# Optimization experiments

Measured on AMD Instinct MI355X. Metric: run time of the kernel, lower is better.

The kernel has to match this reference:

```python
import jax, jax.numpy as jnp
import numpy as np

H = 224          # image height (self.shape[0])
W_IMG = 224      # image width (self.shape[1])
CELLS = 7        # mask_generator num_cells
PAD = CELLS // 2 # reflect pad size
D = 512          # encoder feature dim
NUM_BATCHES = 30
BATCH = 100
EPS = 1e-8       # torch CosineSimilarity eps


def _encode(xb, Wenc):
    # stand-in encoder: 32x32 block average pool -> [B,3,7,7] -> linear to D
    B = xb.shape[0]
    feats = xb.reshape(B, 3, CELLS, H // CELLS, CELLS, W_IMG // CELLS).mean(axis=(3, 5))
    return feats.reshape(B, -1) @ Wenc  # [B, D]


def _cosine(a, b):
    # a: [1,D] (h_star), b: [B,D]; matches nn.CosineSimilarity(dim=1)
    num = jnp.sum(a * b, axis=1)
    den = jnp.maximum(jnp.linalg.norm(a, axis=1) * jnp.linalg.norm(b, axis=1), EPS)
    return num / den  # [B]


def _make_masks(grid, sx, sy):
    # grid: [B,1,7,7] binary floats; bilinear upsample, reflect pad, shifted crop
    B = grid.shape[0]
    up = jax.image.resize(grid, (B, 1, H, W_IMG), method='linear')
    padded = jnp.pad(up, ((0, 0), (0, 0), (PAD, PAD), (PAD, PAD)), mode='reflect')
    crop = jax.vmap(
        lambda g, i, j: jax.lax.dynamic_slice(g, (0, i, j), (1, H, W_IMG))
    )(padded, sx, sy)
    return crop  # [B,1,H,W]


def _relax(x, Wenc, grids, shifts_x, shifts_y):
    h_star = _encode(x, Wenc)  # [1, D]
    R0 = jnp.zeros((H, W_IMG), jnp.float32)
    U0 = jnp.zeros_like(R0)
    sow0 = jnp.full((H, W_IMG), 1e-10, jnp.float32)

    def sample_step(carry, inp):
        # sequential weighted running-mean / Welford variance update
        R, U, sow = carry
        s, m = inp  # s: scalar sim, m: [H,W] mask
        sow = sow + m
        R_new = R + m * (s - R) / sow
        U = U + (s - R_new) * (s - R) * m
        return (R_new, U, sow), None

    def batch_step(carry, binp):
        grid, sx, sy = binp
        masks = _make_masks(grid, sx, sy)        # [B,1,H,W]
        x_mask = x * masks                       # fill_vals_zeros=True path
        h = _encode(x_mask, Wenc)                # [B,D]
        sims = _cosine(h_star, h)                # [B]
        carry, _ = jax.lax.scan(sample_step, carry, (sims, masks[:, 0]))
        return carry, None

    (R, U, sow), _ = jax.lax.scan(batch_step, (R0, U0, sow0),
                                  (grids, shifts_x, shifts_y))
    uncertainty = U / (sow - 1.0)
    return jnp.stack([R, uncertainty])  # [2,H,W]: importance, uncertainty


def setup_inputs() -> dict:
    key = jax.random.key(0)
    k1, k2, k3, k4, k5 = jax.random.split(key, 5)
    x = jax.random.normal(k1, (1, 3, H, W_IMG), jnp.float32)
    Wenc = jax.random.normal(k2, (3 * CELLS * CELLS, D), jnp.float32) * 0.05
    grids = (jax.random.uniform(k3, (NUM_BATCHES, BATCH, 1, CELLS, CELLS)) < 0.5).astype(jnp.float32)
    shifts_x = jax.random.randint(k4, (NUM_BATCHES, BATCH), 0, CELLS)
    shifts_y = jax.random.randint(k5, (NUM_BATCHES, BATCH), 0, CELLS)
    return {"x": x, "Wenc": Wenc, "grids": grids,
            "shifts_x": shifts_x, "shifts_y": shifts_y}


def reference(x, Wenc, grids, shifts_x, shifts_y):
    return _relax(x, Wenc, grids, shifts_x, shifts_y)
```

## Files before the change

### kernel.cpp

```cpp
#include <hip/hip_runtime.h>
#include <math.h>

#define NS 3000
#define NF 147
#define ND 512
#define NSIG 49
#define NSAMP 4
#define NHBLK 750
#define NBLK_VT 1029

#define OFF_WT     0
#define OFF_FEATS  6272
#define OFF_T      236928
#define OFF_G      589952

__device__ __forceinline__ void wt_compute(int sigma, int p, int& i0c, int& i1c,
                                           float& w0, float& w1) {
  int k = p + sigma - 3;
  int r = k < 0 ? -k : (k > 223 ? 446 - k : k);
  float tc = (float)(2 * r - 31) * (1.0f / 64.0f);
  float fl = floorf(tc);
  int i0 = (int)fl;
  float fr = tc - fl;
  i0c = min(max(i0, 0), 6);
  i1c = min(max(i0 + 1, 0), 6);
  w0 = 1.0f - fr;
  w1 = fr;
}

__global__ void __launch_bounds__(256) k_VT(const float* __restrict__ x,
                                            float* __restrict__ ws) {
  int b = blockIdx.x;
  int t = threadIdx.x;
  if (b >= NBLK_VT) {
    if (b == NBLK_VT) {
      float4* WT = (float4*)(ws + OFF_WT);
      for (int e = t; e < 7 * 224; e += 256) {
        int sigma = e / 224, p = e % 224;
        int i0c, i1c; float w0, w1;
        wt_compute(sigma, p, i0c, i1c, w0, w1);
        WT[e] = make_float4(w0, w1, __int_as_float(i0c), __int_as_float(i1c));
      }
    } else {
      int e = (b - NBLK_VT - 1) * 256 + t;
      if (e < 3 * 2401) ws[OFF_G + e] = 0.f;
    }
    return;
  }

  __shared__ float sX[32][33];
  __shared__ float sV[32][8];
  __shared__ float4 sWX[32];
  __shared__ float4 sWY[7][32];
  __shared__ float red[4];

  int f = b % NF;
  int sy = b / NF;
  int c = f / 49, rem = f % 49, cy = rem / 7, cx = rem % 7;

  const float* xb = x + (c * 224 + cy * 32) * 224 + cx * 32;
  float psum = 0.f;
  for (int idx = t; idx < 1024; idx += 256) {
    int yy = idx >> 5, xx = idx & 31;
    float v = xb[yy * 224 + xx];
    sX[yy][xx] = v;
    psum += v;
  }

  if (t < 32) {
    int i0, i1; float w0, w1;
    wt_compute(sy, cx * 32 + t, i0, i1, w0, w1);
    sWX[t] = make_float4(w0, w1, __int_as_float(i0), __int_as_float(i1));
  } else if (t < 32 + 224) {
    int e = t - 32;
    int sx = e >> 5, y0 = e & 31;
    int i0, i1; float w0, w1;
    wt_compute(sx, cy * 32 + y0, i0, i1, w0, w1);
    sWY[sx][y0] = make_float4(w0, w1, __int_as_float(i0), __int_as_float(i1));
  }

  if (sy == 0) {
    float acc = psum;
    for (int off = 32; off; off >>= 1) acc += __shfl_down(acc, off);
    int wave = t >> 6, lane = t & 63;
    if (lane == 0) red[wave] = acc;
  }
  __syncthreads();
  if (sy == 0 && t == 0)
    ws[OFF_FEATS + f] = (red[0] + red[1] + red[2] + red[3]) * (1.0f / 1024.0f);

  if (t < 224) {
    int y0 = t / 7, gx = t % 7;
    float acc = 0.f;
    #pragma unroll
    for (int x0 = 0; x0 < 32; ++x0) {
      float4 wt = sWX[x0];
      int i0 = __float_as_int(wt.z), i1 = __float_as_int(wt.w);
      float w = (gx == i0 ? wt.x : 0.f) + (gx == i1 ? wt.y : 0.f);
      acc = fmaf(w, sX[y0][x0], acc);
    }
    sV[y0][gx] = acc;
  }
  __syncthreads();

  for (int e = t; e < 343; e += 256) {
    int sx = e / 49, r2 = e % 49, gy = r2 / 7, gx = r2 % 7;
    float acc = 0.f;
    #pragma unroll
    for (int y0 = 0; y0 < 32; ++y0) {
      float4 wt = sWY[sx][y0];
      int i0 = __float_as_int(wt.z), i1 = __float_as_int(wt.w);
      float w = (gy == i0 ? wt.x : 0.f) + (gy == i1 ? wt.y : 0.f);
      acc = fmaf(w, sV[y0][gx], acc);
    }
    ws[OFF_T + ((sx * 7 + sy) * 49 + gy * 7 + gx) * NF + f] = acc * (1.0f / 1024.0f);
  }
}

__global__ void __launch_bounds__(256) k_H2s(const float* __restrict__ Wenc,
                                             const float* __restrict__ grids,
                                             const int* __restrict__ shx,
                                             const int* __restrict__ shy,
                                             float* __restrict__ ws) {
  __shared__ __align__(16) float sF[NF * NSAMP];
  __shared__ float sGr[NSAMP * 49];
  __shared__ float sFeat[NF];
  __shared__ int   sSig[NSAMP];
  __shared__ float sRed[2][NSAMP][4];
  __shared__ float sRedH[4];
  __shared__ float sS[NSAMP];
  int t = threadIdx.x;
  int b = blockIdx.x;
  int i0s = b * NSAMP;
  for (int e = t; e < NSAMP * 49; e += 256) sGr[e] = grids[i0s * 49 + e];
  if (t < NSAMP) sSig[t] = shx[i0s + t] * 7 + shy[i0s + t];
  if (t < NF) sFeat[t] = ws[OFF_FEATS + t];
  __syncthreads();
  for (int idx = t; idx < NF * NSAMP; idx += 256) {
    int r = idx / NF, f = idx - r * NF;
    const float* T2 = ws + OFF_T + sSig[r] * (49 * NF) + f;
    const float* gr = sGr + r * 49;
    float acc = 0.f;
    #pragma unroll
    for (int g = 0; g < 49; ++g) acc = fmaf(T2[g * NF], gr[g], acc);
    sF[f * NSAMP + r] = acc;
  }
  __syncthreads();
  float accA[NSAMP], accB[NSAMP];
  #pragma unroll
  for (int r = 0; r < NSAMP; ++r) { accA[r] = 0.f; accB[r] = 0.f; }
  float h0 = 0.f, h1 = 0.f;
  const float2* W2 = (const float2*)Wenc;
  const float4* sF4 = (const float4*)sF;
  for (int f = 0; f < NF; ++f) {
    float2 w = W2[f * (ND / 2) + t];
    float fe = sFeat[f];
    h0 = fmaf(fe, w.x, h0);
    h1 = fmaf(fe, w.y, h1);
    float4 a4 = sF4[f];
    float a[NSAMP] = {a4.x, a4.y, a4.z, a4.w};
    #pragma unroll
    for (int r = 0; r < NSAMP; ++r) {
      accA[r] = fmaf(a[r], w.x, accA[r]);
      accB[r] = fmaf(a[r], w.y, accB[r]);
    }
  }
  int wave = t >> 6, lane = t & 63;
  float hq = h0 * h0 + h1 * h1;
  for (int off = 32; off; off >>= 1) hq += __shfl_down(hq, off);
  if (lane == 0) sRedH[wave] = hq;
  #pragma unroll
  for (int r = 0; r < NSAMP; ++r) {
    float np = accA[r] * h0 + accB[r] * h1;
    float sp = accA[r] * accA[r] + accB[r] * accB[r];
    for (int off = 32; off; off >>= 1) {
      np += __shfl_down(np, off);
      sp += __shfl_down(sp, off);
    }
    if (lane == 0) { sRed[0][r][wave] = np; sRed[1][r][wave] = sp; }
  }
  __syncthreads();
  if (t == 0) sRedH[0] = sqrtf(sRedH[0] + sRedH[1] + sRedH[2] + sRedH[3]);
  __syncthreads();
  if (t < NSAMP) {
    float np = sRed[0][t][0] + sRed[0][t][1] + sRed[0][t][2] + sRed[0][t][3];
    float sp = sRed[1][t][0] + sRed[1][t][1] + sRed[1][t][2] + sRed[1][t][3];
    float den = fmaxf(sRedH[0] * sqrtf(sp), 1e-8f);
    sS[t] = np / den;
  }
  __syncthreads();
  for (int e = t; e < NSAMP * 3 * 49; e += 256) {
    int k = e % 49;
    int rp = e / 49;
    int r = rp / 3, p = rp - r * 3;
    float gv = sGr[r * 49 + k];
    if (gv != 0.f) {
      float s = sS[r];
      float add = (p == 0) ? 1.f : ((p == 1) ? s : s * s);
      atomicAdd(&ws[OFF_G + p * 2401 + sSig[r] * 49 + k], add);
    }
  }
}

__global__ void __launch_bounds__(256) k_CO(const float* __restrict__ ws,
                                            float* __restrict__ out) {
  __shared__ float Gl[3 * 2401];
  __shared__ float sC[NF];
  int b = blockIdx.x;
  int t = threadIdx.x;
  for (int e = t; e < 3 * 2401; e += 256) Gl[e] = ws[OFF_G + e];
  __syncthreads();
  const float4* WT = (const float4*)(ws + OFF_WT);
  if (t < NF) {
    int k = t / 49, r = t - k * 49;
    int sx = r / 7, gy = r % 7;
    float acc = 0.f;
    for (int sy = 0; sy < 7; ++sy) {
      float4 wt = WT[sy * 224 + b];
      int i0 = __float_as_int(wt.z), i1 = __float_as_int(wt.w);
      int base = k * 2401 + (sx * 7 + sy) * 49 + gy * 7;
      acc += wt.x * Gl[base + i0] + wt.y * Gl[base + i1];
    }
    sC[t] = acc;
  }
  __syncthreads();
  if (t < 224) {
    int py = t;
    float S0 = 0.f, S1 = 0.f, S2 = 0.f;
    for (int sx = 0; sx < 7; ++sx) {
      float4 wt = WT[sx * 224 + py];
      int i0 = __float_as_int(wt.z), i1 = __float_as_int(wt.w);
      int base = sx * 7;
      S0 += wt.x * sC[base + i0]      + wt.y * sC[base + i1];
      S1 += wt.x * sC[49 + base + i0] + wt.y * sC[49 + base + i1];
      S2 += wt.x * sC[98 + base + i0] + wt.y * sC[98 + base + i1];
    }
    float W = 1e-10f + S0;
    float R = S1 / W;
    float U = S2 - S1 * S1 / W;
    out[py * 224 + b] = R;
    out[224 * 224 + py * 224 + b] = U / (W - 1.0f);
  }
}

extern "C" void kernel_launch(void* const* d_in, const int* in_sizes, int n_in,
                              void* d_out, int out_size, void* d_ws, size_t ws_size,
                              hipStream_t stream) {
  const float* x     = (const float*)d_in[0];
  const float* Wenc  = (const float*)d_in[1];
  const float* grids = (const float*)d_in[2];
  const int*   shx   = (const int*)d_in[3];
  const int*   shy   = (const int*)d_in[4];
  float* out = (float*)d_out;
  float* ws  = (float*)d_ws;

  k_VT<<<NBLK_VT + 1 + 29, 256, 0, stream>>>(x, ws);
  k_H2s<<<NHBLK, 256, 0, stream>>>(Wenc, grids, shx, shy, ws);
  k_CO<<<224, 256, 0, stream>>>(ws, out);
}
```

Baseline: 101.5 us.

## Use Gram matrix of Wenc for cosine sims and bucket samples by shift

Cosine similarities are now computed from the 147-dimensional pooled features and a precomputed Gram matrix M = Wenc·Wencᵀ, built in extra blocks of the first kernel. This replaces the per-sample 512-wide projection onto Wenc. A counting sort groups samples by shift index, so each 8-sample block usually shares one shift and can merge its atomic accumulations into one add per cell. The price is extra blocks in the first kernel, an O(NF²) load per block, and some precision risk because the norms are formed algebraically from M.

```diff
diff --git a/kernel.cpp b/kernel.cpp
--- a/kernel.cpp
+++ b/kernel.cpp
@@ -5,14 +5,16 @@
 #define NF 147
 #define ND 512
 #define NSIG 49
-#define NSAMP 4
-#define NHBLK 750
+#define NSAMP 8
+#define NHBLK 375
 #define NBLK_VT 1029
 
 #define OFF_WT     0
 #define OFF_FEATS  6272
 #define OFF_T      236928
 #define OFF_G      589952
+#define OFF_M      598016
+#define OFF_ORD    619648
 
 __device__ __forceinline__ void wt_compute(int sigma, int p, int& i0c, int& i1c,
                                            float& w0, float& w1) {
@@ -29,7 +31,18 @@
 }
 
 __global__ void __launch_bounds__(256) k_VT(const float* __restrict__ x,
+                                            const float* __restrict__ Wenc,
+                                            const int* __restrict__ shx,
+                                            const int* __restrict__ shy,
                                             float* __restrict__ ws) {
+  __shared__ float sX[32][33];
+  __shared__ float sV[32][8];
+  __shared__ float4 sWX[32];
+  __shared__ float4 sWY[7][32];
+  __shared__ float red[4];
+  __shared__ float sA[16][33], sB[16][33];
+  __shared__ int hist[64];
+
   int b = blockIdx.x;
   int t = threadIdx.x;
   if (b >= NBLK_VT) {
@@ -41,18 +54,52 @@
         wt_compute(sigma, p, i0c, i1c, w0, w1);
         WT[e] = make_float4(w0, w1, __int_as_float(i0c), __int_as_float(i1c));
       }
-    } else {
+    } else if (b <= NBLK_VT + 29) {
       int e = (b - NBLK_VT - 1) * 256 + t;
       if (e < 3 * 2401) ws[OFF_G + e] = 0.f;
+    } else if (b == NBLK_VT + 30) {
+      if (t < 49) hist[t] = 0;
+      __syncthreads();
+      for (int i = t; i < NS; i += 256)
+        atomicAdd(&hist[shx[i] * 7 + shy[i]], 1);
+      __syncthreads();
+      if (t == 0) {
+        int run = 0;
+        for (int s2 = 0; s2 < 49; ++s2) { int c2 = hist[s2]; hist[s2] = run; run += c2; }
+      }
+      __syncthreads();
+      int* ord = (int*)ws + OFF_ORD;
+      for (int i = t; i < NS; i += 256) {
+        int s2 = shx[i] * 7 + shy[i];
+        ord[atomicAdd(&hist[s2], 1)] = i;
+      }
+    } else {
+      int mm = b - (NBLK_VT + 31);
+      int bi = 0;
+      while (mm >= 10 - bi) { mm -= 10 - bi; ++bi; }
+      int bj = bi + mm;
+      int ti = t >> 4, tj = t & 15;
+      float acc = 0.f;
+      for (int d0 = 0; d0 < ND; d0 += 32) {
+        for (int e = t; e < 512; e += 256) {
+          int r = e >> 5, cc = e & 31;
+          int ia = bi * 16 + r, ja = bj * 16 + r;
+          sA[r][cc] = (ia < NF) ? Wenc[ia * ND + d0 + cc] : 0.f;
+          sB[r][cc] = (ja < NF) ? Wenc[ja * ND + d0 + cc] : 0.f;
+        }
+        __syncthreads();
+        #pragma unroll
+        for (int dd = 0; dd < 32; ++dd) acc = fmaf(sA[ti][dd], sB[tj][dd], acc);
+        __syncthreads();
+      }
+      int i = bi * 16 + ti, j = bj * 16 + tj;
+      if (i < NF && j < NF) {
+        ws[OFF_M + i * NF + j] = acc;
+        if (bi != bj) ws[OFF_M + j * NF + i] = acc;
+      }
     }
     return;
   }
-
-  __shared__ float sX[32][33];
-  __shared__ float sV[32][8];
-  __shared__ float4 sWX[32];
-  __shared__ float4 sWY[7][32];
-  __shared__ float red[4];
 
   int f = b % NF;
   int sy = b / NF;
@@ -117,87 +164,111 @@
   }
 }
 
-__global__ void __launch_bounds__(256) k_H2s(const float* __restrict__ Wenc,
-                                             const float* __restrict__ grids,
+__global__ void __launch_bounds__(256) k_H2s(const float* __restrict__ grids,
                                              const int* __restrict__ shx,
                                              const int* __restrict__ shy,
                                              float* __restrict__ ws) {
-  __shared__ __align__(16) float sF[NF * NSAMP];
-  __shared__ float sGr[NSAMP * 49];
-  __shared__ float sFeat[NF];
+  __shared__ float sF[NSAMP + 1][NF];
+  __shared__ float sGr[NSAMP][49];
   __shared__ int   sSig[NSAMP];
-  __shared__ float sRed[2][NSAMP][4];
-  __shared__ float sRedH[4];
+  __shared__ int   sId[NSAMP];
+  __shared__ float sRed[2 * NSAMP + 1][4];
   __shared__ float sS[NSAMP];
+  __shared__ int   sUni;
   int t = threadIdx.x;
   int b = blockIdx.x;
   int i0s = b * NSAMP;
-  for (int e = t; e < NSAMP * 49; e += 256) sGr[e] = grids[i0s * 49 + e];
-  if (t < NSAMP) sSig[t] = shx[i0s + t] * 7 + shy[i0s + t];
-  if (t < NF) sFeat[t] = ws[OFF_FEATS + t];
+  const int* ord = (const int*)ws + OFF_ORD;
+  if (t < NSAMP) {
+    int id = ord[i0s + t];
+    sId[t] = id;
+    sSig[t] = shx[id] * 7 + shy[id];
+  }
+  if (t < NF) sF[NSAMP][t] = ws[OFF_FEATS + t];
+  __syncthreads();
+  for (int e = t; e < NSAMP * 49; e += 256) {
+    int r = e / 49, k = e % 49;
+    sGr[r][k] = grids[sId[r] * 49 + k];
+  }
+  if (t == 0) {
+    int u = 1;
+    for (int r = 1; r < NSAMP; ++r) u &= (sSig[r] == sSig[0]);
+    sUni = u;
+  }
   __syncthreads();
   for (int idx = t; idx < NF * NSAMP; idx += 256) {
     int r = idx / NF, f = idx - r * NF;
     const float* T2 = ws + OFF_T + sSig[r] * (49 * NF) + f;
-    const float* gr = sGr + r * 49;
+    const float* gr = sGr[r];
     float acc = 0.f;
     #pragma unroll
     for (int g = 0; g < 49; ++g) acc = fmaf(T2[g * NF], gr[g], acc);
-    sF[f * NSAMP + r] = acc;
-  }
-  __syncthreads();
-  float accA[NSAMP], accB[NSAMP];
+    sF[r][f] = acc;
+  }
+  __syncthreads();
+  int tcl = (t < NF) ? t : 0;
+  float msk = (t < NF) ? 1.f : 0.f;
+  const float* Mcol = ws + OFF_M + ((t < NF) ? t : NF - 1);
+  float q[NSAMP + 1];
   #pragma unroll
-  for (int r = 0; r < NSAMP; ++r) { accA[r] = 0.f; accB[r] = 0.f; }
-  float h0 = 0.f, h1 = 0.f;
-  const float2* W2 = (const float2*)Wenc;
-  const float4* sF4 = (const float4*)sF;
-  for (int f = 0; f < NF; ++f) {
-    float2 w = W2[f * (ND / 2) + t];
-    float fe = sFeat[f];
-    h0 = fmaf(fe, w.x, h0);
-    h1 = fmaf(fe, w.y, h1);
-    float4 a4 = sF4[f];
-    float a[NSAMP] = {a4.x, a4.y, a4.z, a4.w};
+  for (int r = 0; r <= NSAMP; ++r) q[r] = 0.f;
+  #pragma unroll 7
+  for (int j = 0; j < NF; ++j) {
+    float mv = Mcol[j * NF];
     #pragma unroll
-    for (int r = 0; r < NSAMP; ++r) {
-      accA[r] = fmaf(a[r], w.x, accA[r]);
-      accB[r] = fmaf(a[r], w.y, accB[r]);
-    }
+    for (int r = 0; r <= NSAMP; ++r) q[r] = fmaf(mv, sF[r][j], q[r]);
   }
   int wave = t >> 6, lane = t & 63;
-  float hq = h0 * h0 + h1 * h1;
-  for (int off = 32; off; off >>= 1) hq += __shfl_down(hq, off);
-  if (lane == 0) sRedH[wave] = hq;
+  float ft = msk * sF[NSAMP][tcl];
   #pragma unroll
   for (int r = 0; r < NSAMP; ++r) {
-    float np = accA[r] * h0 + accB[r] * h1;
-    float sp = accA[r] * accA[r] + accB[r] * accB[r];
+    float pn = q[r] * ft;
+    float pd = msk * q[r] * sF[r][tcl];
     for (int off = 32; off; off >>= 1) {
-      np += __shfl_down(np, off);
-      sp += __shfl_down(sp, off);
-    }
-    if (lane == 0) { sRed[0][r][wave] = np; sRed[1][r][wave] = sp; }
-  }
-  __syncthreads();
-  if (t == 0) sRedH[0] = sqrtf(sRedH[0] + sRedH[1] + sRedH[2] + sRedH[3]);
+      pn += __shfl_down(pn, off);
+      pd += __shfl_down(pd, off);
+    }
+    if (lane == 0) { sRed[r][wave] = pn; sRed[NSAMP + r][wave] = pd; }
+  }
+  {
+    float ph = q[NSAMP] * ft;
+    for (int off = 32; off; off >>= 1) ph += __shfl_down(ph, off);
+    if (lane == 0) sRed[2 * NSAMP][wave] = ph;
+  }
   __syncthreads();
   if (t < NSAMP) {
-    float np = sRed[0][t][0] + sRed[0][t][1] + sRed[0][t][2] + sRed[0][t][3];
-    float sp = sRed[1][t][0] + sRed[1][t][1] + sRed[1][t][2] + sRed[1][t][3];
-    float den = fmaxf(sRedH[0] * sqrtf(sp), 1e-8f);
-    sS[t] = np / den;
-  }
-  __syncthreads();
-  for (int e = t; e < NSAMP * 3 * 49; e += 256) {
-    int k = e % 49;
-    int rp = e / 49;
-    int r = rp / 3, p = rp - r * 3;
-    float gv = sGr[r * 49 + k];
-    if (gv != 0.f) {
-      float s = sS[r];
-      float add = (p == 0) ? 1.f : ((p == 1) ? s : s * s);
-      atomicAdd(&ws[OFF_G + p * 2401 + sSig[r] * 49 + k], add);
+    float num = sRed[t][0] + sRed[t][1] + sRed[t][2] + sRed[t][3];
+    float dq  = sRed[NSAMP + t][0] + sRed[NSAMP + t][1] + sRed[NSAMP + t][2] + sRed[NSAMP + t][3];
+    float hs  = sRed[2 * NSAMP][0] + sRed[2 * NSAMP][1] + sRed[2 * NSAMP][2] + sRed[2 * NSAMP][3];
+    dq = fmaxf(dq, 0.f);
+    hs = fmaxf(hs, 0.f);
+    sS[t] = num / fmaxf(sqrtf(hs) * sqrtf(dq), 1e-8f);
+  }
+  __syncthreads();
+  if (sUni) {
+    for (int e = t; e < 3 * 49; e += 256) {
+      int k = e % 49, p = e / 49;
+      float acc = 0.f;
+      #pragma unroll
+      for (int r = 0; r < NSAMP; ++r) {
+        float gv = sGr[r][k];
+        float s = sS[r];
+        float add = (p == 0) ? 1.f : ((p == 1) ? s : s * s);
+        acc += (gv != 0.f) ? add : 0.f;
+      }
+      if (acc != 0.f) atomicAdd(&ws[OFF_G + p * 2401 + sSig[0] * 49 + k], acc);
+    }
+  } else {
+    for (int e = t; e < NSAMP * 3 * 49; e += 256) {
+      int k = e % 49;
+      int rp = e / 49;
+      int r = rp / 3, p = rp - r * 3;
+      float gv = sGr[r][k];
+      if (gv != 0.f) {
+        float s = sS[r];
+        float add = (p == 0) ? 1.f : ((p == 1) ? s : s * s);
+        atomicAdd(&ws[OFF_G + p * 2401 + sSig[r] * 49 + k], add);
+      }
     }
   }
 }
@@ -254,7 +325,7 @@
   float* out = (float*)d_out;
   float* ws  = (float*)d_ws;
 
-  k_VT<<<NBLK_VT + 1 + 29, 256, 0, stream>>>(x, ws);
-  k_H2s<<<NHBLK, 256, 0, stream>>>(Wenc, grids, shx, shy, ws);
+  k_VT<<<NBLK_VT + 31 + 55, 256, 0, stream>>>(x, Wenc, shx, shy, ws);
+  k_H2s<<<NHBLK, 256, 0, stream>>>(grids, shx, shy, ws);
   k_CO<<<224, 256, 0, stream>>>(ws, out);
 }
```

After: 123.7 us. +21.9%, slower.

## Relayout T table to padded per-feature rows and precompute dense interpolation weights

Applied to the files above, without the earlier changes.

The intermediate table T is stored row-contiguous per (sigma, feature), padded to 52 floats, so k_H2s can read each 49-tap dot product with float4 vector loads instead of strided scalar loads. In k_VT the bilinear weights are expanded into dense per-cell rows in shared memory, so the two small contractions become float4 dot products without per-tap index compares. This adds workspace padding and more shared-memory weight setup per block. The grid-zero blocks also move in the workspace, and the k_VT launch size is unchanged (1029+30 equals 1029+1+29).

```diff
diff --git a/kernel.cpp b/kernel.cpp
--- a/kernel.cpp
+++ b/kernel.cpp
@@ -8,11 +8,12 @@
 #define NSAMP 4
 #define NHBLK 750
 #define NBLK_VT 1029
+#define TROW 52
 
 #define OFF_WT     0
 #define OFF_FEATS  6272
 #define OFF_T      236928
-#define OFF_G      589952
+#define OFF_G      611584
 
 __device__ __forceinline__ void wt_compute(int sigma, int p, int& i0c, int& i1c,
                                            float& w0, float& w1) {
@@ -30,6 +31,12 @@
 
 __global__ void __launch_bounds__(256) k_VT(const float* __restrict__ x,
                                             float* __restrict__ ws) {
+  __shared__ __align__(16) float sX[32][36];
+  __shared__ __align__(16) float sVt[7][36];
+  __shared__ __align__(16) float sWXd[7][36];
+  __shared__ __align__(16) float sWYd[7][7][36];
+  __shared__ float red[4];
+
   int b = blockIdx.x;
   int t = threadIdx.x;
   if (b >= NBLK_VT) {
@@ -48,12 +55,6 @@
     return;
   }
 
-  __shared__ float sX[32][33];
-  __shared__ float sV[32][8];
-  __shared__ float4 sWX[32];
-  __shared__ float4 sWY[7][32];
-  __shared__ float red[4];
-
   int f = b % NF;
   int sy = b / NF;
   int c = f / 49, rem = f % 49, cy = rem / 7, cx = rem % 7;
@@ -67,16 +68,17 @@
     psum += v;
   }
 
-  if (t < 32) {
+  if (t < 224) {
+    int gx = t >> 5, x0 = t & 31;
     int i0, i1; float w0, w1;
-    wt_compute(sy, cx * 32 + t, i0, i1, w0, w1);
-    sWX[t] = make_float4(w0, w1, __int_as_float(i0), __int_as_float(i1));
-  } else if (t < 32 + 224) {
-    int e = t - 32;
-    int sx = e >> 5, y0 = e & 31;
+    wt_compute(sy, cx * 32 + x0, i0, i1, w0, w1);
+    sWXd[gx][x0] = (gx == i0 ? w0 : 0.f) + (gx == i1 ? w1 : 0.f);
+  }
+  for (int e = t; e < 7 * 7 * 32; e += 256) {
+    int sx = e / 224, r2 = e % 224, gy = r2 >> 5, y0 = r2 & 31;
     int i0, i1; float w0, w1;
     wt_compute(sx, cy * 32 + y0, i0, i1, w0, w1);
-    sWY[sx][y0] = make_float4(w0, w1, __int_as_float(i0), __int_as_float(i1));
+    sWYd[sx][gy][y0] = (gy == i0 ? w0 : 0.f) + (gy == i1 ? w1 : 0.f);
   }
 
   if (sy == 0) {
@@ -91,29 +93,35 @@
 
   if (t < 224) {
     int y0 = t / 7, gx = t % 7;
-    float acc = 0.f;
-    #pragma unroll
-    for (int x0 = 0; x0 < 32; ++x0) {
-      float4 wt = sWX[x0];
-      int i0 = __float_as_int(wt.z), i1 = __float_as_int(wt.w);
-      float w = (gx == i0 ? wt.x : 0.f) + (gx == i1 ? wt.y : 0.f);
-      acc = fmaf(w, sX[y0][x0], acc);
-    }
-    sV[y0][gx] = acc;
+    const float4* wrow = (const float4*)sWXd[gx];
+    const float4* xrow = (const float4*)sX[y0];
+    float acc = 0.f;
+    #pragma unroll
+    for (int x4 = 0; x4 < 8; ++x4) {
+      float4 w = wrow[x4], v = xrow[x4];
+      acc = fmaf(w.x, v.x, fmaf(w.y, v.y, fmaf(w.z, v.z, fmaf(w.w, v.w, acc))));
+    }
+    sVt[gx][y0] = acc;
   }
   __syncthreads();
 
   for (int e = t; e < 343; e += 256) {
     int sx = e / 49, r2 = e % 49, gy = r2 / 7, gx = r2 % 7;
-    float acc = 0.f;
-    #pragma unroll
-    for (int y0 = 0; y0 < 32; ++y0) {
-      float4 wt = sWY[sx][y0];
-      int i0 = __float_as_int(wt.z), i1 = __float_as_int(wt.w);
-      float w = (gy == i0 ? wt.x : 0.f) + (gy == i1 ? wt.y : 0.f);
-      acc = fmaf(w, sV[y0][gx], acc);
-    }
-    ws[OFF_T + ((sx * 7 + sy) * 49 + gy * 7 + gx) * NF + f] = acc * (1.0f / 1024.0f);
+    const float4* wrow = (const float4*)sWYd[sx][gy];
+    const float4* vrow = (const float4*)sVt[gx];
+    float acc = 0.f;
+    #pragma unroll
+    for (int y4 = 0; y4 < 8; ++y4) {
+      float w = 0.f;
+      float4 w4 = wrow[y4], v4 = vrow[y4];
+      (void)w;
+      acc = fmaf(w4.x, v4.x, fmaf(w4.y, v4.y, fmaf(w4.z, v4.z, fmaf(w4.w, v4.w, acc))));
+    }
+    ws[OFF_T + ((sx * 7 + sy) * NF + f) * TROW + gy * 7 + gx] = acc * (1.0f / 1024.0f);
+  }
+  if (t < 21) {
+    int sx = t / 3, pd = 49 + t % 3;
+    ws[OFF_T + ((sx * 7 + sy) * NF + f) * TROW + pd] = 0.f;
   }
 }
 
@@ -123,7 +131,7 @@
                                              const int* __restrict__ shy,
                                              float* __restrict__ ws) {
   __shared__ __align__(16) float sF[NF * NSAMP];
-  __shared__ float sGr[NSAMP * 49];
+  __shared__ __align__(16) float sGr[NSAMP][56];
   __shared__ float sFeat[NF];
   __shared__ int   sSig[NSAMP];
   __shared__ float sRed[2][NSAMP][4];
@@ -132,17 +140,21 @@
   int t = threadIdx.x;
   int b = blockIdx.x;
   int i0s = b * NSAMP;
-  for (int e = t; e < NSAMP * 49; e += 256) sGr[e] = grids[i0s * 49 + e];
+  for (int e = t; e < NSAMP * 49; e += 256) sGr[e / 49][e % 49] = grids[i0s * 49 + e];
+  if (t < NSAMP * 7) sGr[t / 7][49 + t % 7] = 0.f;
   if (t < NSAMP) sSig[t] = shx[i0s + t] * 7 + shy[i0s + t];
   if (t < NF) sFeat[t] = ws[OFF_FEATS + t];
   __syncthreads();
   for (int idx = t; idx < NF * NSAMP; idx += 256) {
     int r = idx / NF, f = idx - r * NF;
-    const float* T2 = ws + OFF_T + sSig[r] * (49 * NF) + f;
-    const float* gr = sGr + r * 49;
-    float acc = 0.f;
-    #pragma unroll
-    for (int g = 0; g < 49; ++g) acc = fmaf(T2[g * NF], gr[g], acc);
+    const float4* T2 = (const float4*)(ws + OFF_T + (sSig[r] * NF + f) * TROW);
+    const float4* gr = (const float4*)sGr[r];
+    float acc = 0.f;
+    #pragma unroll
+    for (int g4 = 0; g4 < 13; ++g4) {
+      float4 a = T2[g4], g = gr[g4];
+      acc = fmaf(a.x, g.x, fmaf(a.y, g.y, fmaf(a.z, g.z, fmaf(a.w, g.w, acc))));
+    }
     sF[f * NSAMP + r] = acc;
   }
   __syncthreads();
@@ -193,7 +205,7 @@
     int k = e % 49;
     int rp = e / 49;
     int r = rp / 3, p = rp - r * 3;
-    float gv = sGr[r * 49 + k];
+    float gv = sGr[r][k];
     if (gv != 0.f) {
       float s = sS[r];
       float add = (p == 0) ? 1.f : ((p == 1) ? s : s * s);
@@ -254,7 +266,7 @@
   float* out = (float*)d_out;
   float* ws  = (float*)d_ws;
 
-  k_VT<<<NBLK_VT + 1 + 29, 256, 0, stream>>>(x, ws);
+  k_VT<<<NBLK_VT + 30, 256, 0, stream>>>(x, ws);
   k_H2s<<<NHBLK, 256, 0, stream>>>(Wenc, grids, shx, shy, ws);
   k_CO<<<224, 256, 0, stream>>>(ws, out);
 }
```

Result: faster. 98.53 us (-2.9%).
